# Performance work log

Hardware: AMD Instinct MI355X
Metric: run time of the kernel (lower is better)

The kernel has to match this reference:

```python
import jax, jax.numpy as jnp
import numpy as np

MARGIN = 1.0
EPS = 1e-12


def setup_inputs() -> dict:
    key = jax.random.key(0)
    k1, k2, k3 = jax.random.split(key, 3)
    inputs = jax.random.normal(k1, (8192, 128), dtype=jnp.float32)
    targets = jax.random.randint(k2, (8192,), 0, 64, dtype=jnp.int64)
    center = jax.random.normal(k3, (16, 128), dtype=jnp.float32)
    return {"inputs": inputs, "targets": targets, "center": center}


def reference(inputs, targets, center):
    n = inputs.shape[0]
    # pairwise Euclidean distances via ||a||^2 + ||b||^2 - 2 a.b  (matches addmm_ trick)
    sq = jnp.sum(inputs * inputs, axis=1)                      # [n]
    dist2 = sq[:, None] + sq[None, :] - 2.0 * (inputs @ inputs.T)
    dist = jnp.sqrt(jnp.clip(dist2, EPS))                      # [n, n]

    mask = targets[:, None] == targets[None, :]                # same-class mask [n, n]

    # batch-hard mining, fully vectorized (replaces per-row python loops)
    dist_ap = jnp.max(jnp.where(mask, dist, -jnp.inf), axis=1)  # hardest positive
    neg_min = jnp.min(jnp.where(mask, jnp.inf, dist), axis=1)   # hardest negative
    has_neg = jnp.any(~mask, axis=1)
    dist_an = jnp.where(has_neg, neg_min, dist_ap + MARGIN)

    # center augmentation: min over distances to L2-normalized prototypes
    cn = center / jnp.linalg.norm(center, axis=1, keepdims=True)       # [P, d]
    dc = jnp.sqrt(jnp.sum((inputs[:, None, :] - cn[None, :, :]) ** 2, axis=-1))  # [n, P]
    dc = jnp.clip(dc, EPS)
    dist_an = jnp.minimum(dist_an, jnp.min(dc, axis=1))

    # MarginRankingLoss with y=1: mean(relu(dist_ap - dist_an + margin))
    loss = jnp.mean(jnp.maximum(dist_ap - dist_an + MARGIN, 0.0))
    return loss
```

## Files before the change

kernel.cpp:

```cpp
#include <hip/hip_runtime.h>


#define N_ROWS 8192
#define DIM 128
#define KDIM 192
#define ROWB 384
#define NPROTO 16
#define NSTRIP 16
#define NSTAGE 16
#define MARGIN_F 1.0f
#define EPS_F 1e-12f
#define BIAS_F 32768.0f

typedef __attribute__((ext_vector_type(8))) short short8;
typedef __attribute__((ext_vector_type(4))) float float4v;
typedef __attribute__((ext_vector_type(4))) unsigned uint4v;

static __device__ __forceinline__ unsigned f2bf(float f) {
  unsigned u = __float_as_uint(f);
  u += 0x7fffu + ((u >> 16) & 1u);
  return u >> 16;
}

static __device__ __forceinline__ void gload_lds16(const void* g, void* l) {
  __builtin_amdgcn_global_load_lds(
      (const __attribute__((address_space(1))) unsigned*)g,
      (__attribute__((address_space(3))) unsigned*)l, 16, 0, 0);
}

__global__ void prep_kernel(const float* __restrict__ x,
                            const float* __restrict__ center,
                            const int* __restrict__ tgt,
                            char* __restrict__ xbf,
                            float* __restrict__ sq,
                            float* __restrict__ mindc,
                            float* __restrict__ out) {
  __shared__ float scn[NPROTO * DIM];
  int tid = threadIdx.x;
  if (blockIdx.x == 0 && tid == 0) out[0] = 0.0f;
  int rloc = tid >> 4, l = tid & 15;
  {
    float v[8];
    float ss = 0.f;
#pragma unroll
    for (int j = 0; j < 8; ++j) {
      v[j] = center[rloc * DIM + l * 8 + j];
      ss += v[j] * v[j];
    }
#pragma unroll
    for (int m = 1; m < 16; m <<= 1) ss += __shfl_xor(ss, m, 64);
    float inv = 1.0f / sqrtf(ss);
#pragma unroll
    for (int j = 0; j < 8; ++j) scn[rloc * DIM + l * 8 + j] = v[j] * inv;
  }
  __syncthreads();

  int row = blockIdx.x * 16 + rloc;
  float4 v0 = ((const float4*)x)[row * 32 + l * 2];
  float4 v1 = ((const float4*)x)[row * 32 + l * 2 + 1];
  float ss = v0.x * v0.x + v0.y * v0.y + v0.z * v0.z + v0.w * v0.w +
             v1.x * v1.x + v1.y * v1.y + v1.z * v1.z + v1.w * v1.w;
  float dots[NPROTO];
#pragma unroll
  for (int p = 0; p < NPROTO; ++p) {
    const float* c = &scn[p * DIM + l * 8];
    dots[p] = v0.x * c[0] + v0.y * c[1] + v0.z * c[2] + v0.w * c[3] +
              v1.x * c[4] + v1.y * c[5] + v1.z * c[6] + v1.w * c[7];
  }
#pragma unroll
  for (int m = 1; m < 16; m <<= 1) {
    ss += __shfl_xor(ss, m, 64);
#pragma unroll
    for (int p = 0; p < NPROTO; ++p) dots[p] += __shfl_xor(dots[p], m, 64);
  }
  uint4 pk;
  pk.x = f2bf(v0.x) | (f2bf(v0.y) << 16);
  pk.y = f2bf(v0.z) | (f2bf(v0.w) << 16);
  pk.z = f2bf(v1.x) | (f2bf(v1.y) << 16);
  pk.w = f2bf(v1.z) | (f2bf(v1.w) << 16);
  *(uint4*)(xbf + (size_t)row * ROWB + l * 16) = pk;
  int cls = tgt[row];
  if (l < 8) {
    unsigned wv = (cls & 1) ? 0xC3000000u : 0x0000C300u;
    uint4 oh;
    oh.x = ((cls >> 1) == (l * 4 + 0)) ? wv : 0u;
    oh.y = ((cls >> 1) == (l * 4 + 1)) ? wv : 0u;
    oh.z = ((cls >> 1) == (l * 4 + 2)) ? wv : 0u;
    oh.w = ((cls >> 1) == (l * 4 + 3)) ? wv : 0u;
    *(uint4*)(xbf + (size_t)row * ROWB + 256 + l * 16) = oh;
  }
  if (l == 0) {
    float mind2 = INFINITY;
#pragma unroll
    for (int p = 0; p < NPROTO; ++p)
      mind2 = fminf(mind2, ss + 1.0f - 2.0f * dots[p]);
    sq[row] = ss;
    mindc[row] = fmaxf(sqrtf(fmaxf(mind2, 0.0f)), EPS_F);
  }
}

__global__ __launch_bounds__(256, 4) void
pairdist_kernel(const char* __restrict__ xbf, const float* __restrict__ sq,
                float* __restrict__ pmax, float* __restrict__ pmin) {
  __shared__ __align__(16) char bl[2][12288];
  const int bid = blockIdx.x;
  const int rg = bid >> 4;
  const int strip = bid & 15;
  const int wave = threadIdx.x >> 6, lane = threadIdx.x & 63;
  const int q = lane >> 4, l16 = lane & 15;
  const int rowbase = rg * 128 + wave * 32;
  const int stripbase = strip * 512;

  const int slot = threadIdx.x;
  const char* const srcstrip = xbf + (size_t)stripbase * ROWB;
  int soff[3];
#pragma unroll
  for (int r = 0; r < 3; ++r) {
    int o = r * 4096 + slot * 16;
    int c = o / ROWB;
    soff[r] = c * ROWB + ((o - c * ROWB) ^ ((c & 7) << 4));
  }

  auto stage = [&](int s, char* buf) {
    const char* g = srcstrip + (size_t)s * 12288;
#pragma unroll
    for (int r = 0; r < 3; ++r)
      gload_lds16(g + soff[r], buf + r * 4096 + wave * 1024);
  };

  stage(0, bl[0]);

  short8 a[2][6];
#pragma unroll
  for (int rt = 0; rt < 2; ++rt) {
    const char* ar = xbf + (size_t)(rowbase + rt * 16 + l16) * ROWB + q * 16;
#pragma unroll
    for (int kc = 0; kc < 6; ++kc) a[rt][kc] = *(const short8*)(ar + kc * 64);
#pragma unroll
    for (int kc = 4; kc < 6; ++kc) {
      uint4v u = __builtin_bit_cast(uint4v, a[rt][kc]);
      u ^= 0x80008000u;
      a[rt][kc] = __builtin_bit_cast(short8, u);
    }
  }
#pragma unroll
  for (int rt = 0; rt < 2; ++rt)
#pragma unroll
    for (int kc = 0; kc < 6; ++kc)
      asm volatile("" : "+v"(a[rt][kc]));

  int roffb[6];
#pragma unroll
  for (int kc = 0; kc < 6; ++kc)
    roffb[kc] = (l16 * ROWB + kc * 64 + q * 16) ^ ((l16 & 7) << 4);

  float maxp[8], minn[8];
#pragma unroll
  for (int i = 0; i < 8; ++i) { maxp[i] = -INFINITY; minn[i] = INFINITY; }

#pragma unroll 1
  for (int s = 0; s < NSTAGE; ++s) {
    __syncthreads();
    if (s + 1 < NSTAGE) stage(s + 1, bl[(s + 1) & 1]);
    const char* cur = bl[s & 1];
    float sqs[2];
#pragma unroll
    for (int ss = 0; ss < 2; ++ss)
      sqs[ss] = sq[stripbase + s * 32 + ss * 16 + l16];
#pragma unroll
    for (int ss = 0; ss < 2; ++ss) {
      const char* bufp = cur + ss * 6144;
      short8 b[6];
#pragma unroll
      for (int kc = 0; kc < 6; ++kc) b[kc] = *(const short8*)(bufp + roffb[kc]);
      float4v acc[2];
#pragma unroll
      for (int rt = 0; rt < 2; ++rt) acc[rt] = (float4v){0.f, 0.f, 0.f, 0.f};
      __builtin_amdgcn_s_setprio(1);
#pragma unroll
      for (int kc = 0; kc < 6; ++kc)
#pragma unroll
        for (int rt = 0; rt < 2; ++rt)
          acc[rt] = __builtin_amdgcn_mfma_f32_16x16x32_bf16(a[rt][kc], b[kc],
                                                            acc[rt], 0, 0, 0);
      __builtin_amdgcn_s_setprio(0);
#pragma unroll
      for (int rt = 0; rt < 2; ++rt)
#pragma unroll
        for (int r = 0; r < 4; ++r) {
          float v = fmaf(-2.0f, acc[rt][r], sqs[ss]);
          int idx = rt * 4 + r;
          maxp[idx] = fmaxf(maxp[idx], v);
          minn[idx] = fminf(minn[idx], v);
        }
    }
  }

#pragma unroll
  for (int m = 1; m < 16; m <<= 1)
#pragma unroll
    for (int i = 0; i < 8; ++i) {
      maxp[i] = fmaxf(maxp[i], __shfl_xor(maxp[i], m, 64));
      minn[i] = fminf(minn[i], __shfl_xor(minn[i], m, 64));
    }
  if (l16 == 0) {
    float* pM = pmax + (size_t)strip * N_ROWS + rowbase + q * 4;
    float* pm = pmin + (size_t)strip * N_ROWS + rowbase + q * 4;
#pragma unroll
    for (int rt = 0; rt < 2; ++rt)
#pragma unroll
      for (int r = 0; r < 4; ++r) {
        pM[rt * 16 + r] = maxp[rt * 4 + r];
        pm[rt * 16 + r] = minn[rt * 4 + r];
      }
  }
}

__global__ void finalize_kernel(const float* __restrict__ pmax,
                                const float* __restrict__ pmin,
                                const float* __restrict__ sq,
                                const float* __restrict__ mindc,
                                float* __restrict__ out) {
  __shared__ float wsum[4];
  int i = blockIdx.x * 256 + threadIdx.x;
  float maxv = -INFINITY, minv = INFINITY;
#pragma unroll
  for (int s = 0; s < NSTRIP; ++s) {
    maxv = fmaxf(maxv, pmax[s * N_ROWS + i]);
    minv = fminf(minv, pmin[s * N_ROWS + i]);
  }
  float si = sq[i];
  float dap = sqrtf(fmaxf(si + (maxv - BIAS_F), EPS_F));
  float dan = (minv > 16384.0f) ? (dap + MARGIN_F)
                                : sqrtf(fmaxf(si + minv, EPS_F));
  dan = fminf(dan, mindc[i]);
  float c = fmaxf(dap - dan + MARGIN_F, 0.0f) * (1.0f / (float)N_ROWS);
#pragma unroll
  for (int m = 1; m < 64; m <<= 1) c += __shfl_xor(c, m, 64);
  int lane = threadIdx.x & 63, wv = threadIdx.x >> 6;
  if (lane == 0) wsum[wv] = c;
  __syncthreads();
  if (threadIdx.x == 0) atomicAdd(out, wsum[0] + wsum[1] + wsum[2] + wsum[3]);
}

extern "C" void kernel_launch(void* const* d_in, const int* in_sizes, int n_in,
                              void* d_out, int out_size, void* d_ws, size_t ws_size,
                              hipStream_t stream) {
  const float* inputs = (const float*)d_in[0];
  const int* targets = (const int*)d_in[1];
  const float* center = (const float*)d_in[2];
  char* ws = (char*)d_ws;
  char* xbf    = ws;
  float* sq    = (float*)(ws + 3145728);
  float* mindc = (float*)(ws + 3178496);
  float* pmax  = (float*)(ws + 3211264);
  float* pmin  = (float*)(ws + 3735552);
  float* out   = (float*)d_out;

  prep_kernel<<<512, 256, 0, stream>>>(inputs, center, targets, xbf, sq, mindc, out);
  pairdist_kernel<<<1024, 256, 0, stream>>>(xbf, sq, pmax, pmin);
  finalize_kernel<<<32, 256, 0, stream>>>(pmax, pmin, sq, mindc, out);
}
```

Before: 91.87 us.

## Triple-buffer LDS stages with explicit vmcnt waits and stage sq into LDS

Moves the B-operand staging from a double buffer to a triple buffer with two stages in flight. Each iteration waits only on the older stage's loads, using an explicit s_waitcnt vmcnt(3) plus a barrier instead of __syncthreads, which drained every outstanding load. The strip's squared norms are loaded into LDS once at the start rather than read from global memory every stage. The cost is more LDS per block (three 12 KB buffers plus 2 KB), which may limit blocks per CU. The hand-written vmcnt counts depend on the exact number of loads each wave issues, so a miscount would be a correctness risk.

Measured after the change: 95.12 us. +3.5%, slower.

```diff
diff --git a/kernel.cpp b/kernel.cpp
--- a/kernel.cpp
+++ b/kernel.cpp
@@ -102,12 +102,11 @@
 __global__ __launch_bounds__(256, 4) void
 pairdist_kernel(const char* __restrict__ xbf, const float* __restrict__ sq,
                 float* __restrict__ pmax, float* __restrict__ pmin) {
-  __shared__ __align__(16) char bl[2][12288];
-  const int bid = blockIdx.x;
-  const int rg = bid >> 4;
-  const int strip = bid & 15;
+  __shared__ __align__(16) char bl[3][12288];
+  __shared__ __align__(16) float sqlds[512];
   const int wave = threadIdx.x >> 6, lane = threadIdx.x & 63;
   const int q = lane >> 4, l16 = lane & 15;
+  const int rg = blockIdx.x >> 4, strip = blockIdx.x & 15;
   const int rowbase = rg * 128 + wave * 32;
   const int stripbase = strip * 512;
 
@@ -128,8 +127,6 @@
       gload_lds16(g + soff[r], buf + r * 4096 + wave * 1024);
   };
 
-  stage(0, bl[0]);
-
   short8 a[2][6];
 #pragma unroll
   for (int rt = 0; rt < 2; ++rt) {
@@ -149,6 +146,12 @@
     for (int kc = 0; kc < 6; ++kc)
       asm volatile("" : "+v"(a[rt][kc]));
 
+  if (wave < 2)
+    gload_lds16((const char*)(sq + stripbase) + wave * 1024 + lane * 16,
+                (char*)sqlds + wave * 1024 + lane * 16);
+  stage(0, bl[0]);
+  stage(1, bl[1]);
+
   int roffb[6];
 #pragma unroll
   for (int kc = 0; kc < 6; ++kc)
@@ -158,21 +161,22 @@
 #pragma unroll
   for (int i = 0; i < 8; ++i) { maxp[i] = -INFINITY; minn[i] = INFINITY; }
 
+  asm volatile("s_waitcnt vmcnt(3)" ::: "memory");
+  __builtin_amdgcn_s_barrier();
+  asm volatile("" ::: "memory");
+
 #pragma unroll 1
   for (int s = 0; s < NSTAGE; ++s) {
-    __syncthreads();
-    if (s + 1 < NSTAGE) stage(s + 1, bl[(s + 1) & 1]);
-    const char* cur = bl[s & 1];
-    float sqs[2];
-#pragma unroll
-    for (int ss = 0; ss < 2; ++ss)
-      sqs[ss] = sq[stripbase + s * 32 + ss * 16 + l16];
-#pragma unroll
-    for (int ss = 0; ss < 2; ++ss) {
-      const char* bufp = cur + ss * 6144;
+    if (s + 2 < NSTAGE) stage(s + 2, bl[(s + 2) % 3]);
+    const char* cur = bl[s % 3];
+#pragma unroll
+    for (int p = 0; p < 2; ++p) {
+      const char* bufp = cur + p * 6144;
+      float sqc = sqlds[s * 32 + p * 16 + l16];
       short8 b[6];
 #pragma unroll
-      for (int kc = 0; kc < 6; ++kc) b[kc] = *(const short8*)(bufp + roffb[kc]);
+      for (int kc = 0; kc < 6; ++kc)
+        b[kc] = *(const short8*)(bufp + roffb[kc]);
       float4v acc[2];
 #pragma unroll
       for (int rt = 0; rt < 2; ++rt) acc[rt] = (float4v){0.f, 0.f, 0.f, 0.f};
@@ -188,11 +192,19 @@
       for (int rt = 0; rt < 2; ++rt)
 #pragma unroll
         for (int r = 0; r < 4; ++r) {
-          float v = fmaf(-2.0f, acc[rt][r], sqs[ss]);
+          float v = fmaf(-2.0f, acc[rt][r], sqc);
           int idx = rt * 4 + r;
           maxp[idx] = fmaxf(maxp[idx], v);
           minn[idx] = fminf(minn[idx], v);
         }
+    }
+    if (s < NSTAGE - 1) {
+      if (s + 2 < NSTAGE)
+        asm volatile("s_waitcnt vmcnt(3)" ::: "memory");
+      else
+        asm volatile("s_waitcnt vmcnt(0)" ::: "memory");
+      __builtin_amdgcn_s_barrier();
+      asm volatile("" ::: "memory");
     }
   }
 
```
